# Kernel optimization log

Hardware: AMD Instinct MI355X
Metric: run time of the kernel (lower is better)

The kernel has to match this reference:

```python
import jax, jax.numpy as jnp
import numpy as np

ALPHA = 0.5  # init alpha
B, T, D, H = 32, 1024, 512, 512


def _cell(x, h, c, wih, whh, bih, bhh):
    # PyTorch LSTM cell: gates in i, f, g, o order
    g = x @ wih.T + bih + h @ whh.T + bhh  # (B, 4H)
    i, f, gg, o = jnp.split(g, 4, axis=-1)
    c2 = jax.nn.sigmoid(f) * c + jax.nn.sigmoid(i) * jnp.tanh(gg)
    h2 = jax.nn.sigmoid(o) * jnp.tanh(c2)
    return h2, c2


def setup_inputs() -> dict:
    key = jax.random.key(0)
    ks = jax.random.split(key, 9)
    s = 1.0 / np.sqrt(H)  # torch default init scale
    u = lambda k, shp: jax.random.uniform(k, shp, jnp.float32, -s, s)
    return {
        "u_sequence": jax.random.normal(ks[0], (B, T, D), jnp.float32),
        "w_ih_f": u(ks[1], (4 * H, D)),
        "w_hh_f": u(ks[2], (4 * H, H)),
        "b_ih_f": u(ks[3], (4 * H,)),
        "b_hh_f": u(ks[4], (4 * H,)),
        "w_ih_b": u(ks[5], (4 * H, D)),
        "w_hh_b": u(ks[6], (4 * H, H)),
        "b_ih_b": u(ks[7], (4 * H,)),
        "b_hh_b": u(ks[8], (4 * H,)),
    }


def reference(u_sequence, w_ih_f, w_hh_f, b_ih_f, b_hh_f,
              w_ih_b, w_hh_b, b_ih_b, b_hh_b):
    # Per timestep the original calls the bidirectional LSTM on a length-1
    # slice: both directions reduce to a single cell step on the same input.
    # Hidden/cell state (2, B, H) is carried across timesteps.
    pf = (w_ih_f, w_hh_f, b_ih_f, b_hh_f)
    pb = (w_ih_b, w_hh_b, b_ih_b, b_hh_b)
    Bn, Tn, Dn = u_sequence.shape
    Hn = w_hh_f.shape[1]
    z = jnp.zeros((Bn, Hn), u_sequence.dtype)

    def bi_step(x, hf, cf, hb, cb):
        hf2, cf2 = _cell(x, hf, cf, *pf)
        hb2, cb2 = _cell(x, hb, cb, *pb)
        # lstm_out[:, 0, :] == concat(h_fwd, h_bwd) for seq_len == 1
        return jnp.concatenate([hf2, hb2], axis=-1), hf2, cf2, hb2, cb2

    def step(carry, u_t):  # u_t: (B, D)
        hf, cf, hb, cb = carry
        out1, hf1, cf1, hb1, cb1 = bi_step(u_t, hf, cf, hb, cb)
        x_hat = out1[:, -1:]                 # last channel scalar, (B, 1)
        x_hat_prime = u_t + x_hat            # broadcast -> (B, D)
        out2, hf2, cf2, hb2, cb2 = bi_step(x_hat_prime, hf1, cf1, hb1, cb1)
        x_hat_next = out2[:, -1:]
        out = u_t + (1.0 - ALPHA) * x_hat_prime + ALPHA * x_hat_next
        return (hf2, cf2, hb2, cb2), out

    u_tm = jnp.swapaxes(u_sequence, 0, 1)    # (T, B, D)
    _, outs = jax.lax.scan(step, (z, z, z, z), u_tm)
    return jnp.swapaxes(outs, 0, 1)          # (B, T, D)
```

## Files before the change

### kernel.cpp

```cpp
#include <hip/hip_runtime.h>
#include <cstdint>
#include <cstddef>

#define BB 32
#define TT 1024
#define DD 512
#define HH 512
#define NBLK 128

typedef __bf16 bf16x8 __attribute__((ext_vector_type(8)));
typedef float  f32x4  __attribute__((ext_vector_type(4)));
typedef unsigned long long u64;

#define HFRAG_OFF 0
#define XHAT_OFF  131072
#define IFLAG_OFF 393216
#define GCNT_OFF  394240

#define AT_LOAD(p)     __hip_atomic_load((p),      __ATOMIC_RELAXED, __HIP_MEMORY_SCOPE_AGENT)
#define AT_STORE(p, v) __hip_atomic_store((p), (v), __ATOMIC_RELAXED, __HIP_MEMORY_SCOPE_AGENT)

__device__ __forceinline__ float sigm(float x) {
    return 1.f / (1.f + __expf(-x));
}
__device__ __forceinline__ float tanh_fast(float x) {
    x = fminf(15.f, fmaxf(-15.f, x));
    float e = __expf(2.f * x);
    return (e - 1.f) / (e + 1.f);
}


__device__ __forceinline__ void arrive_flag(int* iflags, int bid) {
    __builtin_amdgcn_s_waitcnt(0);
    __syncthreads();
    if (threadIdx.x == 0) AT_STORE(&iflags[bid], 1);
}
__device__ __forceinline__ void wait_flag(const int* iflags) {
    if (threadIdx.x < 64) {
        const u64* f64 = (const u64*)iflags;
        for (;;) {
            u64 a = AT_LOAD(&f64[threadIdx.x]);
            bool ok = ((int)a >= 1) & ((int)(a >> 32) >= 1);
            if (__all(ok)) break;
            __builtin_amdgcn_s_sleep(1);
        }
    }
    __syncthreads();
}

__device__ __forceinline__ void arrive_cnt(int* gcnt, int bid) {
    __builtin_amdgcn_s_waitcnt(0);
    __syncthreads();
    if (threadIdx.x == 0)
        __hip_atomic_fetch_add(&gcnt[(bid & 7) * 16], 1,
                               __ATOMIC_RELAXED, __HIP_MEMORY_SCOPE_AGENT);
}
__device__ __forceinline__ void wait_cnt(const int* gcnt, int target) {
    if (threadIdx.x < 64) {
        const int* p = &gcnt[(threadIdx.x & 7) * 16];
        for (;;) {
            int v = AT_LOAD(p);
            if (__all(v >= target)) break;
        }
    }
    __syncthreads();
}

__global__ __launch_bounds__(256, 1) void lstm_persistent(
    const float* __restrict__ u,
    const float* __restrict__ wih_f, const float* __restrict__ whh_f,
    const float* __restrict__ bih_f, const float* __restrict__ bhh_f,
    const float* __restrict__ wih_b, const float* __restrict__ whh_b,
    const float* __restrict__ bih_b, const float* __restrict__ bhh_b,
    unsigned short* __restrict__ hfrag, float* __restrict__ xhat,
    int* __restrict__ iflags, int* __restrict__ gcnt)
{
    const int bid  = blockIdx.x;
    const int dir  = bid >> 6;
    const int kb   = bid & 63;
    const int k0   = kb << 3;
    const int tid  = threadIdx.x;
    const int wid  = tid >> 6;
    const int mi   = wid >> 1;
    const int ni   = wid & 1;
    const int lane = tid & 63;
    const int quad = lane >> 4;
    const int l16  = lane & 15;

    const float* wih = dir ? wih_b : wih_f;
    const float* whh = dir ? whh_b : whh_f;
    const float* bih = dir ? bih_b : bih_f;
    const float* bhh = dir ? bhh_b : bhh_f;

    bf16x8 wihF[16], whhF[16];
    {
        const int jg = (l16 >> 2) * HH + (k0 + 4 * mi) + (l16 & 3);
        #pragma unroll
        for (int s = 0; s < 16; ++s) {
            const float* p = wih + (size_t)jg * DD + s * 32 + quad * 8;
            const float* q = whh + (size_t)jg * HH + s * 32 + quad * 8;
            bf16x8 a, b;
            #pragma unroll
            for (int i = 0; i < 8; ++i) { a[i] = (__bf16)p[i]; b[i] = (__bf16)q[i]; }
            wihF[s] = a;
            whhF[s] = b;
        }
    }

    const int kc = k0 + 4 * mi + quad;
    const int bc = ni * 16 + l16;

    float rsv[4], biasv[4];
    {
        float rs = 0.f;
        #pragma unroll
        for (int s = 0; s < 16; ++s)
            #pragma unroll
            for (int i = 0; i < 8; ++i) rs += (float)wihF[s][i];
        rs += __shfl_xor(rs, 16);
        rs += __shfl_xor(rs, 32);
        #pragma unroll
        for (int g = 0; g < 4; ++g) {
            rsv[g]   = __shfl(rs, g * 4 + quad);
            const int j = g * HH + kc;
            biasv[g] = bih[j] + bhh[j];
        }
    }

    const int sw = kc >> 5, qw = (kc >> 3) & 3, iw = kc & 7;
    const int lanew = qw * 16 + l16;
    unsigned* hfrag32 = (unsigned*)hfrag;
    const int ws32_0 = (((((dir * 2 + 0) * 2 + ni) * 16 + sw) * 64 + lanew) * 8 + iw) >> 1;
    const int ws32_1 = ws32_0 + (2 * 16 * 64 * 8 >> 1);
    const u64* h64 = (const u64*)hfrag;
    const int rbA = ((dir * 2 + 0) * 2 + ni) * 2048 + lane * 2;
    const int rbB = ((dir * 2 + 1) * 2 + ni) * 2048 + lane * 2;

    if (!(quad & 1)) AT_STORE(&hfrag32[ws32_0], 0u);
    if (bid == 0 && tid < 8) AT_STORE(&gcnt[tid * 16], 0);

    __shared__ __align__(16) float gbuf[4][16][20];

    auto ugemm = [&](int t) -> f32x4 {
        f32x4 a0 = (f32x4){0.f, 0.f, 0.f, 0.f};
        f32x4 a1 = (f32x4){0.f, 0.f, 0.f, 0.f};
        const float* ub = u + (size_t)bc * (TT * DD) + (size_t)t * DD + quad * 8;
        #pragma unroll
        for (int s = 0; s < 16; ++s) {
            const float4* p = (const float4*)(ub + s * 32);
            float4 x0 = p[0], x1 = p[1];
            bf16x8 uf;
            uf[0] = (__bf16)x0.x; uf[1] = (__bf16)x0.y;
            uf[2] = (__bf16)x0.z; uf[3] = (__bf16)x0.w;
            uf[4] = (__bf16)x1.x; uf[5] = (__bf16)x1.y;
            uf[6] = (__bf16)x1.z; uf[7] = (__bf16)x1.w;
            if (s & 1) a1 = __builtin_amdgcn_mfma_f32_16x16x32_bf16(wihF[s], uf, a1, 0, 0, 0);
            else       a0 = __builtin_amdgcn_mfma_f32_16x16x32_bf16(wihF[s], uf, a0, 0, 0, 0);
        }
        return a0 + a1;
    };

    arrive_flag(iflags, bid);
    f32x4 gih = ugemm(0);
    wait_flag(iflags);

    float c = 0.f;
    f32x4 gnext = gih;
    int n = 1;

    for (int t = 0; t < TT; ++t) {
        #pragma unroll 1
        for (int pass = 0; pass < 2; ++pass, ++n) {
            const int bufR = (t * 2 + pass) & 1;
            float xc = 0.f;
            if (pass) xc = AT_LOAD(&xhat[t * BB + bc]);

            u64 ha[16], hb[16];
            {
                const int rb = bufR ? rbB : rbA;
                #pragma unroll
                for (int s = 0; s < 16; ++s) {
                    ha[s] = AT_LOAD(&h64[rb + s * 128]);
                    hb[s] = AT_LOAD(&h64[rb + s * 128 + 1]);
                }
            }
            f32x4 acc0 = gih;
            f32x4 acc1 = (f32x4){0.f, 0.f, 0.f, 0.f};
            #pragma unroll
            for (int s = 0; s < 16; ++s) {
                union { u64 q[2]; bf16x8 v; } cvt;
                cvt.q[0] = ha[s]; cvt.q[1] = hb[s];
                if (s & 1) acc1 = __builtin_amdgcn_mfma_f32_16x16x32_bf16(whhF[s], cvt.v, acc1, 0, 0, 0);
                else       acc0 = __builtin_amdgcn_mfma_f32_16x16x32_bf16(whhF[s], cvt.v, acc0, 0, 0, 0);
            }
            f32x4 acc = acc0 + acc1;

            float4 gw; gw.x = acc[0]; gw.y = acc[1]; gw.z = acc[2]; gw.w = acc[3];
            *(float4*)&gbuf[wid][l16][quad * 4] = gw;
            __syncthreads();
            float gI = gbuf[wid][l16][ 0 + quad] + biasv[0] + xc * rsv[0];
            float gF = gbuf[wid][l16][ 4 + quad] + biasv[1] + xc * rsv[1];
            float gG = gbuf[wid][l16][ 8 + quad] + biasv[2] + xc * rsv[2];
            float gO = gbuf[wid][l16][12 + quad] + biasv[3] + xc * rsv[3];

            float ig = sigm(gI), fg = sigm(gF), gg = tanh_fast(gG), og = sigm(gO);
            c = fg * c + ig * gg;
            float h = og * tanh_fast(c);

            float hp = __shfl_xor(h, 16);
            if (dir == 1 && kc == (HH - 1))
                AT_STORE(&xhat[pass * (TT * BB) + t * BB + bc], h);
            if (!(quad & 1)) {
                unsigned lo = (unsigned)__builtin_bit_cast(unsigned short, (__bf16)h);
                unsigned hi = (unsigned)__builtin_bit_cast(unsigned short, (__bf16)hp);
                AT_STORE(&hfrag32[bufR ? ws32_0 : ws32_1], lo | (hi << 16));
            }

            arrive_cnt(gcnt, bid);
            if (pass == 1 && t + 1 < TT)
                gnext = ugemm(t + 1);
            wait_cnt(gcnt, 16 * n);
        }
        gih = gnext;
    }
}

__global__ void epilogue(const float* __restrict__ u, const float* __restrict__ xhat,
                         float* __restrict__ out)
{
    const int i = blockIdx.x * blockDim.x + threadIdx.x;
    const float4 uv = ((const float4*)u)[i];
    const int bt = i >> 7;
    const int t = bt & (TT - 1);
    const int b = bt >> 10;
    const float s = 0.5f * (xhat[t * BB + b] + xhat[TT * BB + t * BB + b]);
    float4 o;
    o.x = 1.5f * uv.x + s;
    o.y = 1.5f * uv.y + s;
    o.z = 1.5f * uv.z + s;
    o.w = 1.5f * uv.w + s;
    ((float4*)out)[i] = o;
}

extern "C" void kernel_launch(void* const* d_in, const int* in_sizes, int n_in,
                              void* d_out, int out_size, void* d_ws, size_t ws_size,
                              hipStream_t stream) {
    const float* u     = (const float*)d_in[0];
    const float* wih_f = (const float*)d_in[1];
    const float* whh_f = (const float*)d_in[2];
    const float* bih_f = (const float*)d_in[3];
    const float* bhh_f = (const float*)d_in[4];
    const float* wih_b = (const float*)d_in[5];
    const float* whh_b = (const float*)d_in[6];
    const float* bih_b = (const float*)d_in[7];
    const float* bhh_b = (const float*)d_in[8];

    char* ws = (char*)d_ws;
    unsigned short* hfrag = (unsigned short*)(ws + HFRAG_OFF);
    float* xhat           = (float*)(ws + XHAT_OFF);
    int* iflags           = (int*)(ws + IFLAG_OFF);
    int* gcnt             = (int*)(ws + GCNT_OFF);

    lstm_persistent<<<NBLK, 256, 0, stream>>>(
        u, wih_f, whh_f, bih_f, bhh_f, wih_b, whh_b, bih_b, bhh_b,
        hfrag, xhat, iflags, gcnt);

    const int n4 = BB * TT * DD / 4;
    epilogue<<<n4 / 256, 256, 0, stream>>>(u, xhat, (float*)d_out);
}
```

Before: 15.54 ms.

## Merge directions into 64 blocks, use per-block version flags, split input GEMM across passes

```diff
diff --git a/kernel.cpp b/kernel.cpp
--- a/kernel.cpp
+++ b/kernel.cpp
@@ -6,7 +6,8 @@
 #define TT 1024
 #define DD 512
 #define HH 512
-#define NBLK 128
+#define NBLK 64
+#define NTHR 512
 
 typedef __bf16 bf16x8 __attribute__((ext_vector_type(8)));
 typedef float  f32x4  __attribute__((ext_vector_type(4)));
@@ -15,7 +16,7 @@
 #define HFRAG_OFF 0
 #define XHAT_OFF  131072
 #define IFLAG_OFF 393216
-#define GCNT_OFF  394240
+#define VFLAG_OFF 394240
 
 #define AT_LOAD(p)     __hip_atomic_load((p),      __ATOMIC_RELAXED, __HIP_MEMORY_SCOPE_AGENT)
 #define AT_STORE(p, v) __hip_atomic_store((p), (v), __ATOMIC_RELAXED, __HIP_MEMORY_SCOPE_AGENT)
@@ -37,51 +38,63 @@
 }
 __device__ __forceinline__ void wait_flag(const int* iflags) {
     if (threadIdx.x < 64) {
-        const u64* f64 = (const u64*)iflags;
         for (;;) {
-            u64 a = AT_LOAD(&f64[threadIdx.x]);
-            bool ok = ((int)a >= 1) & ((int)(a >> 32) >= 1);
-            if (__all(ok)) break;
+            int v = AT_LOAD(&iflags[threadIdx.x]);
+            if (__all(v >= 1)) break;
             __builtin_amdgcn_s_sleep(1);
         }
     }
     __syncthreads();
 }
 
-__device__ __forceinline__ void arrive_cnt(int* gcnt, int bid) {
+__device__ __forceinline__ void publish(int* vf, int bid, int n) {
     __builtin_amdgcn_s_waitcnt(0);
     __syncthreads();
-    if (threadIdx.x == 0)
-        __hip_atomic_fetch_add(&gcnt[(bid & 7) * 16], 1,
-                               __ATOMIC_RELAXED, __HIP_MEMORY_SCOPE_AGENT);
-}
-__device__ __forceinline__ void wait_cnt(const int* gcnt, int target) {
+    if (threadIdx.x == 0) AT_STORE(&vf[bid], n);
+}
+__device__ __forceinline__ void wait_ver(const int* vf, int n) {
     if (threadIdx.x < 64) {
-        const int* p = &gcnt[(threadIdx.x & 7) * 16];
         for (;;) {
-            int v = AT_LOAD(p);
-            if (__all(v >= target)) break;
-        }
-    }
-    __syncthreads();
-}
-
-__global__ __launch_bounds__(256, 1) void lstm_persistent(
+            int v = AT_LOAD(&vf[threadIdx.x]);
+            if (__all(v >= n)) break;
+        }
+    }
+    __syncthreads();
+}
+
+#define UGEMM_HALF(tt, S0)                                                    \
+  {                                                                           \
+    const float* ub = u + (size_t)bc * (TT * DD) + (size_t)(tt) * DD + quad * 8; \
+    _Pragma("unroll")                                                         \
+    for (int i8 = 0; i8 < 8; ++i8) {                                          \
+      const int s = (S0) + i8;                                                \
+      const float4* p = (const float4*)(ub + s * 32);                         \
+      float4 x0 = p[0], x1 = p[1];                                            \
+      bf16x8 uf;                                                              \
+      uf[0] = (__bf16)x0.x; uf[1] = (__bf16)x0.y;                             \
+      uf[2] = (__bf16)x0.z; uf[3] = (__bf16)x0.w;                             \
+      uf[4] = (__bf16)x1.x; uf[5] = (__bf16)x1.y;                             \
+      uf[6] = (__bf16)x1.z; uf[7] = (__bf16)x1.w;                             \
+      if (s & 1) un1 = __builtin_amdgcn_mfma_f32_16x16x32_bf16(wihF[s], uf, un1, 0, 0, 0); \
+      else       un0 = __builtin_amdgcn_mfma_f32_16x16x32_bf16(wihF[s], uf, un0, 0, 0, 0); \
+    }                                                                         \
+  }
+
+__global__ __launch_bounds__(NTHR, 1) void lstm_persistent(
     const float* __restrict__ u,
     const float* __restrict__ wih_f, const float* __restrict__ whh_f,
     const float* __restrict__ bih_f, const float* __restrict__ bhh_f,
     const float* __restrict__ wih_b, const float* __restrict__ whh_b,
     const float* __restrict__ bih_b, const float* __restrict__ bhh_b,
     unsigned short* __restrict__ hfrag, float* __restrict__ xhat,
-    int* __restrict__ iflags, int* __restrict__ gcnt)
+    int* __restrict__ iflags, int* __restrict__ vflags)
 {
     const int bid  = blockIdx.x;
-    const int dir  = bid >> 6;
-    const int kb   = bid & 63;
-    const int k0   = kb << 3;
+    const int k0   = bid << 3;
     const int tid  = threadIdx.x;
     const int wid  = tid >> 6;
-    const int mi   = wid >> 1;
+    const int dir  = wid >> 2;
+    const int mi   = (wid >> 1) & 1;
     const int ni   = wid & 1;
     const int lane = tid & 63;
     const int quad = lane >> 4;
@@ -137,35 +150,19 @@
     const int rbB = ((dir * 2 + 1) * 2 + ni) * 2048 + lane * 2;
 
     if (!(quad & 1)) AT_STORE(&hfrag32[ws32_0], 0u);
-    if (bid == 0 && tid < 8) AT_STORE(&gcnt[tid * 16], 0);
-
-    __shared__ __align__(16) float gbuf[4][16][20];
-
-    auto ugemm = [&](int t) -> f32x4 {
-        f32x4 a0 = (f32x4){0.f, 0.f, 0.f, 0.f};
-        f32x4 a1 = (f32x4){0.f, 0.f, 0.f, 0.f};
-        const float* ub = u + (size_t)bc * (TT * DD) + (size_t)t * DD + quad * 8;
-        #pragma unroll
-        for (int s = 0; s < 16; ++s) {
-            const float4* p = (const float4*)(ub + s * 32);
-            float4 x0 = p[0], x1 = p[1];
-            bf16x8 uf;
-            uf[0] = (__bf16)x0.x; uf[1] = (__bf16)x0.y;
-            uf[2] = (__bf16)x0.z; uf[3] = (__bf16)x0.w;
-            uf[4] = (__bf16)x1.x; uf[5] = (__bf16)x1.y;
-            uf[6] = (__bf16)x1.z; uf[7] = (__bf16)x1.w;
-            if (s & 1) a1 = __builtin_amdgcn_mfma_f32_16x16x32_bf16(wihF[s], uf, a1, 0, 0, 0);
-            else       a0 = __builtin_amdgcn_mfma_f32_16x16x32_bf16(wihF[s], uf, a0, 0, 0, 0);
-        }
-        return a0 + a1;
-    };
+    if (bid == 0 && tid < 64) AT_STORE(&vflags[tid], 0);
+
+    __shared__ __align__(16) float gbuf[8][16][20];
 
     arrive_flag(iflags, bid);
-    f32x4 gih = ugemm(0);
+    f32x4 un0 = (f32x4){0.f, 0.f, 0.f, 0.f};
+    f32x4 un1 = (f32x4){0.f, 0.f, 0.f, 0.f};
+    UGEMM_HALF(0, 0);
+    UGEMM_HALF(0, 8);
     wait_flag(iflags);
 
+    f32x4 gih = un0 + un1;
     float c = 0.f;
-    f32x4 gnext = gih;
     int n = 1;
 
     for (int t = 0; t < TT; ++t) {
@@ -216,12 +213,19 @@
                 AT_STORE(&hfrag32[bufR ? ws32_0 : ws32_1], lo | (hi << 16));
             }
 
-            arrive_cnt(gcnt, bid);
-            if (pass == 1 && t + 1 < TT)
-                gnext = ugemm(t + 1);
-            wait_cnt(gcnt, 16 * n);
-        }
-        gih = gnext;
+            publish(vflags, bid, n);
+            if (t + 1 < TT) {
+                if (pass == 0) {
+                    un0 = (f32x4){0.f, 0.f, 0.f, 0.f};
+                    un1 = (f32x4){0.f, 0.f, 0.f, 0.f};
+                    UGEMM_HALF(t + 1, 0);
+                } else {
+                    UGEMM_HALF(t + 1, 8);
+                }
+            }
+            wait_ver(vflags, n);
+        }
+        gih = un0 + un1;
     }
 }
 
@@ -259,11 +263,11 @@
     unsigned short* hfrag = (unsigned short*)(ws + HFRAG_OFF);
     float* xhat           = (float*)(ws + XHAT_OFF);
     int* iflags           = (int*)(ws + IFLAG_OFF);
-    int* gcnt             = (int*)(ws + GCNT_OFF);
-
-    lstm_persistent<<<NBLK, 256, 0, stream>>>(
+    int* vflags           = (int*)(ws + VFLAG_OFF);
+
+    lstm_persistent<<<NBLK, NTHR, 0, stream>>>(
         u, wih_f, whh_f, bih_f, bhh_f, wih_b, whh_b, bih_b, bhh_b,
-        hfrag, xhat, iflags, gcnt);
+        hfrag, xhat, iflags, vflags);
 
     const int n4 = BB * TT * DD / 4;
     epilogue<<<n4 / 256, 256, 0, stream>>>(u, xhat, (float*)d_out);
```

Measured after the change: 15.28 ms. About the same (-1.7%).
